# Kernel optimization log

Hardware: AMD Instinct MI355X
Metric: run time of the kernel (lower is better)

The kernel has to match this reference:

```python
import jax, jax.numpy as jnp
import numpy as np

B, N = 2048, 1024
GRAVITY = 9.81007
SIG_G2 = (1.6968e-4) ** 2  # default gyro covariance (EuRoC)
SIG_A2 = (2.0e-3) ** 2     # default accel covariance (EuRoC)


def skew(v):
    x, y, z = v[..., 0], v[..., 1], v[..., 2]
    o = jnp.zeros_like(x)
    return jnp.stack([
        jnp.stack([o, -z, y], -1),
        jnp.stack([z, o, -x], -1),
        jnp.stack([-y, x, o], -1)], -2)


def so3_exp(phi):
    # phi [...,3] -> unit quaternion [...,4] (xyzw)
    t2 = jnp.sum(phi * phi, axis=-1, keepdims=True)
    small = t2 < 1e-8
    t = jnp.sqrt(jnp.where(small, 1.0, t2))
    s = jnp.where(small, 0.5 - t2 / 48.0, jnp.sin(0.5 * t) / t)
    w = jnp.where(small, 1.0 - t2 / 8.0, jnp.cos(0.5 * t))
    return jnp.concatenate([phi * s, w], axis=-1)


def so3_Jr(phi):
    # right Jacobian of Exp at phi: I - c1*K + c2*K@K
    t2 = jnp.sum(phi * phi, axis=-1)[..., None, None]
    small = t2 < 1e-8
    t2s = jnp.where(small, 1.0, t2)
    t = jnp.sqrt(t2s)
    c1 = jnp.where(small, 0.5 - t2 / 24.0, (1.0 - jnp.cos(t)) / t2s)
    c2 = jnp.where(small, 1.0 / 6.0 - t2 / 120.0, (t - jnp.sin(t)) / (t2s * t))
    K = skew(phi)
    I = jnp.eye(3, dtype=phi.dtype)
    return I - c1 * K + c2 * (K @ K)


def quat_mul(q, r):
    x1, y1, z1, w1 = q[..., 0], q[..., 1], q[..., 2], q[..., 3]
    x2, y2, z2, w2 = r[..., 0], r[..., 1], r[..., 2], r[..., 3]
    return jnp.stack([
        w1 * x2 + x1 * w2 + y1 * z2 - z1 * y2,
        w1 * y2 - x1 * z2 + y1 * w2 + z1 * x2,
        w1 * z2 + x1 * y2 - y1 * x2 + z1 * w2,
        w1 * w2 - x1 * x2 - y1 * y2 - z1 * z2], -1)


def quat_inv(q):
    return jnp.concatenate([-q[..., :3], q[..., 3:]], -1)


def quat_to_mat(q):
    x, y, z, w = q[..., 0], q[..., 1], q[..., 2], q[..., 3]
    r0 = jnp.stack([1 - 2 * (y * y + z * z), 2 * (x * y - z * w), 2 * (x * z + y * w)], -1)
    r1 = jnp.stack([2 * (x * y + z * w), 1 - 2 * (x * x + z * z), 2 * (y * z - x * w)], -1)
    r2 = jnp.stack([2 * (x * z - y * w), 2 * (y * z + x * w), 1 - 2 * (x * x + y * y)], -1)
    return jnp.stack([r0, r1, r2], -2)


def rotate(q, v):
    return jnp.einsum('...ij,...j->...i', quat_to_mat(q), v)


def setup_inputs() -> dict:
    key = jax.random.key(0)
    k1, k2, k3 = jax.random.split(key, 3)
    dt = jax.random.uniform(k1, (B, N, 1), dtype=jnp.float32) * 0.004 + 0.001  # ~200Hz IMU
    ang = 0.5 * jax.random.normal(k2, (B, N, 3), dtype=jnp.float32)
    acc = jax.random.normal(k3, (B, N, 3), dtype=jnp.float32)
    pos0 = jnp.zeros((B, 3), jnp.float32)
    vel0 = jnp.zeros((B, 3), jnp.float32)
    rot0 = jnp.zeros((B, 4), jnp.float32).at[:, 3].set(1.0)  # identity SO3
    return {"dt": dt, "ang": ang, "acc": acc, "pos0": pos0, "vel0": vel0, "rot0": rot0}


def reference(dt, ang, acc, pos0, vel0, rot0):
    dtype = dt.dtype
    b = pos0.shape[0]
    grav = jnp.array([0.0, 0.0, GRAVITY], dtype=dtype)
    I3 = jnp.eye(3, dtype=dtype)

    def step(carry, x):
        dp, dv, drq, tacc, cov = carry
        dt_k, ang_k, acc_k = x  # [B,1], [B,3], [B,3]
        phi = ang_k * dt_k
        dr = so3_exp(phi)
        # a = acc - (rot0 * dr_ik * dr).Inv() @ gravity
        q_tot = quat_mul(quat_mul(rot0, drq), dr)
        a = acc_k - rotate(quat_inv(q_tot), grav)
        Ra = rotate(drq, a)  # old dR applied to a
        dp_n = dp + dv * dt_k + 0.5 * Ra * dt_k ** 2
        dv_n = dv + Ra * dt_k
        drq_n = quat_mul(drq, dr)
        tacc_n = tacc + dt_k
        # --- covariance propagation (Forster A7-A10) ---
        dtb = dt_k[..., None]             # [B,1,1]
        Rnew = quat_to_mat(drq_n)         # [B,3,3] (code uses updated dR)
        RHa = Rnew @ skew(acc_k)
        Z3 = jnp.zeros_like(RHa)
        E3 = jnp.broadcast_to(I3, RHa.shape)
        drT = jnp.swapaxes(quat_to_mat(dr), -1, -2)
        row0 = jnp.concatenate([drT, Z3, Z3], -1)
        row1 = jnp.concatenate([-RHa * dtb, E3, Z3], -1)
        row2 = jnp.concatenate([-0.5 * RHa * dtb ** 2, E3 * dtb, E3], -1)
        A = jnp.concatenate([row0, row1, row2], -2)  # [B,9,9]
        JrDt = so3_Jr(phi) * dtb
        Bg = jnp.concatenate([JrDt, Z3, Z3], -2)                              # [B,9,3]
        Ba = jnp.concatenate([Z3, Rnew * dtb, 0.5 * Rnew * dtb ** 2], -2)     # [B,9,3]
        cov_n = (A @ cov @ jnp.swapaxes(A, -1, -2)
                 + SIG_G2 * (Bg @ jnp.swapaxes(Bg, -1, -2))
                 + SIG_A2 * (Ba @ jnp.swapaxes(Ba, -1, -2)))
        return (dp_n, dv_n, drq_n, tacc_n, cov_n), None

    init = (jnp.zeros((b, 3), dtype), jnp.zeros((b, 3), dtype),
            jnp.tile(jnp.array([0.0, 0.0, 0.0, 1.0], dtype), (b, 1)),
            jnp.zeros((b, 1), dtype), jnp.zeros((b, 9, 9), dtype))
    xs = (jnp.swapaxes(dt, 0, 1), jnp.swapaxes(ang, 0, 1), jnp.swapaxes(acc, 0, 1))
    (dp, dv, drq, tacc, cov), _ = jax.lax.scan(step, init, xs)

    rot_out = quat_mul(rot0, drq)
    vel_out = vel0 + rotate(rot0, dv)
    pos_out = pos0 + vel0 * tacc + rotate(rot0, dp)
    return rot_out, vel_out, pos_out, cov
```

## Files before the change

### kernel.cpp

```cpp
#include <hip/hip_runtime.h>
#include <math.h>

#define GRAVITY_C 9.81007f
#define SIG_G2_C (1.6968e-4f * 1.6968e-4f)
#define SIG_A2_C (2.0e-3f * 2.0e-3f)

struct Seg {
  float q[4];
  float t;
  float dv[3], dp[3];
  float P10[9], P20[9];
  float c00[6], c01[9], c02[9], c11[6], c12[9], c22[6];
};

static __device__ __forceinline__ void q2m(const float q[4], float R[9]) {
  float x = q[0], y = q[1], z = q[2], w = q[3];
  R[0] = 1.f - 2.f * (y * y + z * z); R[1] = 2.f * (x * y - z * w);       R[2] = 2.f * (x * z + y * w);
  R[3] = 2.f * (x * y + z * w);       R[4] = 1.f - 2.f * (x * x + z * z); R[5] = 2.f * (y * z - x * w);
  R[6] = 2.f * (x * z - y * w);       R[7] = 2.f * (y * z + x * w);       R[8] = 1.f - 2.f * (x * x + y * y);
}

static __device__ __forceinline__ void qmul(const float a[4], const float b[4], float o[4]) {
  float x1 = a[0], y1 = a[1], z1 = a[2], w1 = a[3];
  float x2 = b[0], y2 = b[1], z2 = b[2], w2 = b[3];
  o[0] = w1 * x2 + x1 * w2 + y1 * z2 - z1 * y2;
  o[1] = w1 * y2 - x1 * z2 + y1 * w2 + z1 * x2;
  o[2] = w1 * z2 + x1 * y2 - y1 * x2 + z1 * w2;
  o[3] = w1 * w2 - x1 * x2 - y1 * y2 - z1 * z2;
}

static __device__ __forceinline__ void mm(const float A[9], const float B[9], float C[9]) {
#pragma unroll
  for (int i = 0; i < 3; i++)
#pragma unroll
    for (int j = 0; j < 3; j++)
      C[3 * i + j] = A[3 * i + 0] * B[0 + j] + A[3 * i + 1] * B[3 + j] + A[3 * i + 2] * B[6 + j];
}
static __device__ __forceinline__ void mmT(const float A[9], const float B[9], float C[9]) {
#pragma unroll
  for (int i = 0; i < 3; i++)
#pragma unroll
    for (int j = 0; j < 3; j++)
      C[3 * i + j] = A[3 * i + 0] * B[3 * j + 0] + A[3 * i + 1] * B[3 * j + 1] + A[3 * i + 2] * B[3 * j + 2];
}
static __device__ __forceinline__ void mTm(const float A[9], const float B[9], float C[9]) {
#pragma unroll
  for (int i = 0; i < 3; i++)
#pragma unroll
    for (int j = 0; j < 3; j++)
      C[3 * i + j] = A[0 + i] * B[0 + j] + A[3 + i] * B[3 + j] + A[6 + i] * B[6 + j];
}

static __device__ __forceinline__ void expand6(const float c[6], float f[9]) {
  f[0] = c[0]; f[1] = c[1]; f[2] = c[2];
  f[3] = c[1]; f[4] = c[3]; f[5] = c[4];
  f[6] = c[2]; f[7] = c[4]; f[8] = c[5];
}

__device__ __constant__ const int SI6[6] = {0, 0, 0, 1, 1, 2};
__device__ __constant__ const int SJ6[6] = {0, 1, 2, 1, 2, 2};

static __device__ __forceinline__ void step(Seg& s, float Ro[9], float gb[3], float dtv,
                                            float omx, float omy, float omz,
                                            float acx, float acy, float acz) {
  float px = omx * dtv, py = omy * dtv, pz = omz * dtv;
  float t2 = px * px + py * py + pz * pz;
  float s_ = 0.5f - t2 * (1.0f / 48.0f);
  float qd[4] = {px * s_, py * s_, pz * s_, 1.0f - 0.125f * t2};

  float Rd[9]; q2m(qd, Rd);
  float qn[4]; qmul(s.q, qd, qn);
  float Rn[9]; q2m(qn, Rn);

  float gbn[3];
#pragma unroll
  for (int i = 0; i < 3; i++)
    gbn[i] = Rd[0 + i] * gb[0] + Rd[3 + i] * gb[1] + Rd[6 + i] * gb[2];
  float bx = acx - gbn[0], by = acy - gbn[1], bz = acz - gbn[2];
  float Ra[3];
#pragma unroll
  for (int i = 0; i < 3; i++)
    Ra[i] = Ro[3 * i + 0] * bx + Ro[3 * i + 1] * by + Ro[3 * i + 2] * bz;

  float hdt = 0.5f * dtv;
  float hdt2 = hdt * dtv;
#pragma unroll
  for (int i = 0; i < 3; i++) s.dp[i] += s.dv[i] * dtv + Ra[i] * hdt2;
#pragma unroll
  for (int i = 0; i < 3; i++) s.dv[i] += Ra[i] * dtv;

  float M[9];
#pragma unroll
  for (int i = 0; i < 3; i++) {
    M[3 * i + 0] = -dtv * (Rn[3 * i + 1] * acz - Rn[3 * i + 2] * acy);
    M[3 * i + 1] = -dtv * (-Rn[3 * i + 0] * acz + Rn[3 * i + 2] * acx);
    M[3 * i + 2] = -dtv * (Rn[3 * i + 0] * acy - Rn[3 * i + 1] * acx);
  }

  float TP[9]; mmT(M, Ro, TP);
#pragma unroll
  for (int k = 0; k < 9; k++) s.P20[k] += hdt * TP[k] + dtv * s.P10[k];
#pragma unroll
  for (int k = 0; k < 9; k++) s.P10[k] += TP[k];

  float C00f[9]; expand6(s.c00, C00f);

  float W01[9]; mmT(C00f, TP, W01);
  float Y1h[9]; mm(TP, s.c01, Y1h);
  float Y2h[9]; mm(TP, s.c02, Y2h);

  float Wm6[6];
#pragma unroll
  for (int s6 = 0; s6 < 6; s6++) {
    const int i = SI6[s6], j = SJ6[s6];
    Wm6[s6] = W01[0 + i] * TP[3 * j + 0] + W01[3 + i] * TP[3 * j + 1] + W01[6 + i] * TP[3 * j + 2];
  }
  float WmF[9]; expand6(Wm6, WmF);

#pragma unroll
  for (int k = 0; k < 9; k++) s.c02[k] += hdt * (W01[k] + 2.0f * s.c01[k]);
#pragma unroll
  for (int k = 0; k < 9; k++) s.c01[k] += W01[k];

  {
    float ph[3];
#pragma unroll
    for (int i = 0; i < 3; i++)
      ph[i] = Rn[3 * i + 0] * px + Rn[3 * i + 1] * py + Rn[3 * i + 2] * pz;
    float sgdt2 = SIG_G2_C * dtv * dtv;
    float a_ = sgdt2 * (1.0f - t2 * (1.0f / 12.0f));
    float b_ = sgdt2 * ((1.0f / 12.0f) - t2 * (1.0f / 36.0f));
#pragma unroll
    for (int s6 = 0; s6 < 6; s6++) {
      const int i = SI6[s6], j = SJ6[s6];
      float v = s.c00[s6] + b_ * ph[i] * ph[j];
      if (i == j) v += a_;
      s.c00[s6] = v;
    }
  }

  float C11f[9]; expand6(s.c11, C11f);
  float c11p[9];
#pragma unroll
  for (int i = 0; i < 3; i++)
#pragma unroll
    for (int j = 0; j < 3; j++)
      c11p[3 * i + j] = WmF[3 * i + j] + Y1h[3 * i + j] + Y1h[3 * j + i] + C11f[3 * i + j];

  float c12p[9];
#pragma unroll
  for (int i = 0; i < 3; i++)
#pragma unroll
    for (int j = 0; j < 3; j++)
      c12p[3 * i + j] = hdt * (c11p[3 * i + j] + Y1h[3 * i + j] + C11f[3 * i + j])
                      + Y2h[3 * i + j] + s.c12[3 * i + j];

  float dt2v = dtv * dtv;
  float nh2 = -hdt * hdt;
#pragma unroll
  for (int s6 = 0; s6 < 6; s6++) {
    const int i = SI6[s6], j = SJ6[s6];
    float v = s.c22[s6]
            + hdt * (c12p[3 * i + j] + c12p[3 * j + i] + s.c12[3 * i + j] + s.c12[3 * j + i])
            + nh2 * (c11p[3 * i + j] - C11f[3 * i + j]);
    if (i == j) v += SIG_A2_C * 0.25f * dt2v * dt2v;
    s.c22[s6] = v;
  }
#pragma unroll
  for (int i = 0; i < 3; i++)
#pragma unroll
    for (int j = 0; j < 3; j++) {
      float v = c12p[3 * i + j];
      if (i == j) v += SIG_A2_C * hdt * dt2v;
      s.c12[3 * i + j] = v;
    }
#pragma unroll
  for (int s6 = 0; s6 < 6; s6++) {
    const int i = SI6[s6], j = SJ6[s6];
    float v = c11p[3 * i + j];
    if (i == j) v += SIG_A2_C * dt2v;
    s.c11[s6] = v;
  }

#pragma unroll
  for (int i = 0; i < 4; i++) s.q[i] = qn[i];
#pragma unroll
  for (int k = 0; k < 9; k++) Ro[k] = Rn[k];
#pragma unroll
  for (int i = 0; i < 3; i++) gb[i] = gbn[i];
  s.t += dtv;
}

template <int CNT>
static __device__ __forceinline__ void shsel(const float* v, int d, bool rt, float* X, float* Y) {
#pragma unroll
  for (int i = 0; i < CNT; i++) {
    float o = __shfl_xor(v[i], d, 64);
    X[i] = rt ? o : v[i];
    Y[i] = rt ? v[i] : o;
  }
}

static __device__ __forceinline__ void compose(Seg& s, int d, int lane) {
  bool rt = (lane & d) != 0;

  {
    float xq[4], yq[4];
    shsel<4>(s.q, d, rt, xq, yq);
    qmul(xq, yq, s.q);
  }
  float ot = __shfl_xor(s.t, d, 64);
  float tY = rt ? s.t : ot;
  s.t = s.t + ot;

  {
    float xu[3], yu[3], xw[3], yw[3];
    shsel<3>(s.dv, d, rt, xu, yu);
    shsel<3>(s.dp, d, rt, xw, yw);
#pragma unroll
    for (int i = 0; i < 3; i++) s.dp[i] = xw[i] + tY * xu[i] + yw[i];
#pragma unroll
    for (int i = 0; i < 3; i++) s.dv[i] = xu[i] + yu[i];
  }

  float N1[9], N2[9], xP10[9], xP20[9];
  shsel<9>(s.P10, d, rt, xP10, N1);
  shsel<9>(s.P20, d, rt, xP20, N2);

  float x00[6], y00[6];
  shsel<6>(s.c00, d, rt, x00, y00);
  float X00f[9]; expand6(x00, X00f);
  float K1[9]; mm(N1, X00f, K1);
  float K2[9]; mm(N2, X00f, K2);
#pragma unroll
  for (int s6 = 0; s6 < 6; s6++) s.c00[s6] = x00[s6] + y00[s6];

  float x01[9], y01[9];
  shsel<9>(s.c01, d, rt, x01, y01);
  float L1[9]; mm(N1, x01, L1);
  float L2[9]; mm(N2, x01, L2);
  float x02[9], y02[9];
  shsel<9>(s.c02, d, rt, x02, y02);
  float L3[9]; mm(N1, x02, L3);
  float L4[9]; mm(N2, x02, L4);

#pragma unroll
  for (int i = 0; i < 3; i++)
#pragma unroll
    for (int j = 0; j < 3; j++) {
      s.c01[3 * i + j] = x01[3 * i + j] + K1[3 * j + i] + y01[3 * i + j];
      s.c02[3 * i + j] = x02[3 * i + j] + tY * x01[3 * i + j] + K2[3 * j + i] + y02[3 * i + j];
    }

  float x11[6], y11[6], x12[9], y12[9], x22[6], y22[6];
  shsel<6>(s.c11, d, rt, x11, y11);
  shsel<9>(s.c12, d, rt, x12, y12);
  shsel<6>(s.c22, d, rt, x22, y22);
  float X11f[9]; expand6(x11, X11f);

#pragma unroll
  for (int s6 = 0; s6 < 6; s6++) {
    const int i = SI6[s6], j = SJ6[s6];
    float kn = K1[3 * i + 0] * N1[3 * j + 0] + K1[3 * i + 1] * N1[3 * j + 1] + K1[3 * i + 2] * N1[3 * j + 2];
    s.c11[s6] = x11[s6] + L1[3 * i + j] + L1[3 * j + i] + kn + y11[s6];
  }
#pragma unroll
  for (int i = 0; i < 3; i++)
#pragma unroll
    for (int j = 0; j < 3; j++) {
      float kn = K1[3 * i + 0] * N2[3 * j + 0] + K1[3 * i + 1] * N2[3 * j + 1] + K1[3 * i + 2] * N2[3 * j + 2];
      s.c12[3 * i + j] = x12[3 * i + j] + L3[3 * i + j] + tY * (L1[3 * i + j] + X11f[3 * i + j])
                       + L2[3 * j + i] + kn + y12[3 * i + j];
    }
  float tY2 = tY * tY;
#pragma unroll
  for (int s6 = 0; s6 < 6; s6++) {
    const int i = SI6[s6], j = SJ6[s6];
    float kn = K2[3 * i + 0] * N2[3 * j + 0] + K2[3 * i + 1] * N2[3 * j + 1] + K2[3 * i + 2] * N2[3 * j + 2];
    s.c22[s6] = x22[s6] + kn + L4[3 * i + j] + L4[3 * j + i]
              + tY * (L2[3 * i + j] + L2[3 * j + i] + x12[3 * i + j] + x12[3 * j + i])
              + tY2 * X11f[3 * i + j] + y22[s6];
  }

#pragma unroll
  for (int k = 0; k < 9; k++) s.P20[k] = xP20[k] + tY * xP10[k] + N2[k];
#pragma unroll
  for (int k = 0; k < 9; k++) s.P10[k] = xP10[k] + N1[k];
}

static __device__ __forceinline__ void sandw(const float R[9], float A[9]) {
  float T1[9]; mm(R, A, T1);
  mmT(T1, R, A);
}

__global__ __launch_bounds__(256, 1) void imu_kernel(
    const float* __restrict__ dt, const float* __restrict__ ang, const float* __restrict__ acc,
    const float* __restrict__ pos0, const float* __restrict__ vel0, const float* __restrict__ rot0,
    float* __restrict__ out, int B, int N) {
  int lane = threadIdx.x & 63;
  int wave = threadIdx.x >> 6;
  int b = blockIdx.x * 4 + wave;
  if (b >= B) return;
  int chunk = N >> 6;

  long base = (long)b * N + (long)lane * chunk;
  const float* dtp = dt + base;
  const float* angp = ang + base * 3;
  const float* accp = acc + base * 3;

  float qc[4] = {0.f, 0.f, 0.f, 1.f};
#pragma unroll 1
  for (int jb = 0; jb < (chunk >> 2); ++jb) {
    float4 d4 = *reinterpret_cast<const float4*>(dtp + jb * 4);
    float4 g0 = *reinterpret_cast<const float4*>(angp + jb * 12 + 0);
    float4 g1 = *reinterpret_cast<const float4*>(angp + jb * 12 + 4);
    float4 g2 = *reinterpret_cast<const float4*>(angp + jb * 12 + 8);
    float dd[4] = {d4.x, d4.y, d4.z, d4.w};
    float gg[12] = {g0.x, g0.y, g0.z, g0.w, g1.x, g1.y, g1.z, g1.w, g2.x, g2.y, g2.z, g2.w};
#pragma unroll
    for (int u = 0; u < 4; ++u) {
      float dtv = dd[u];
      float px = gg[3 * u + 0] * dtv, py = gg[3 * u + 1] * dtv, pz = gg[3 * u + 2] * dtv;
      float t2 = px * px + py * py + pz * pz;
      float s_ = 0.5f - t2 * (1.0f / 48.0f);
      float qd[4] = {px * s_, py * s_, pz * s_, 1.0f - 0.125f * t2};
      float qn[4]; qmul(qc, qd, qn);
      qc[0] = qn[0]; qc[1] = qn[1]; qc[2] = qn[2]; qc[3] = qn[3];
    }
  }
#pragma unroll
  for (int d = 1; d < 64; d <<= 1) {
    float o0 = __shfl_up(qc[0], d, 64);
    float o1 = __shfl_up(qc[1], d, 64);
    float o2 = __shfl_up(qc[2], d, 64);
    float o3 = __shfl_up(qc[3], d, 64);
    if (lane >= d) {
      float oq[4] = {o0, o1, o2, o3};
      float nn[4]; qmul(oq, qc, nn);
      qc[0] = nn[0]; qc[1] = nn[1]; qc[2] = nn[2]; qc[3] = nn[3];
    }
  }
  float Q[4];
  Q[0] = __shfl_up(qc[0], 1, 64);
  Q[1] = __shfl_up(qc[1], 1, 64);
  Q[2] = __shfl_up(qc[2], 1, 64);
  Q[3] = __shfl_up(qc[3], 1, 64);
  if (lane == 0) { Q[0] = 0.f; Q[1] = 0.f; Q[2] = 0.f; Q[3] = 1.f; }

  float RQ[9]; q2m(Q, RQ);

  float r0q[4] = {rot0[b * 4 + 0], rot0[b * 4 + 1], rot0[b * 4 + 2], rot0[b * 4 + 3]};
  float g_l[3];
  {
    float R0[9]; q2m(r0q, R0);
    float gp[3] = {R0[6] * GRAVITY_C, R0[7] * GRAVITY_C, R0[8] * GRAVITY_C};
#pragma unroll
    for (int i = 0; i < 3; i++)
      g_l[i] = RQ[0 + i] * gp[0] + RQ[3 + i] * gp[1] + RQ[6 + i] * gp[2];
  }

  Seg s = {};
  s.q[3] = 1.0f;
  float Ro[9] = {1.f, 0.f, 0.f, 0.f, 1.f, 0.f, 0.f, 0.f, 1.f};
  float gb[3] = {g_l[0], g_l[1], g_l[2]};

  float dc = dtp[0];
  float gx = angp[0], gy = angp[1], gz = angp[2];
  float ax = accp[0], ay = accp[1], az = accp[2];
#pragma unroll 1
  for (int j = 0; j < chunk; ++j) {
    int jn = (j + 1 < chunk) ? j + 1 : j;
    float dn = dtp[jn];
    float gnx = angp[3 * jn + 0], gny = angp[3 * jn + 1], gnz = angp[3 * jn + 2];
    float anx = accp[3 * jn + 0], any2 = accp[3 * jn + 1], anz = accp[3 * jn + 2];
    step(s, Ro, gb, dc, gx, gy, gz, ax, ay, az);
    dc = dn; gx = gnx; gy = gny; gz = gnz; ax = anx; ay = any2; az = anz;
  }

  {
    float tv[3];
#pragma unroll
    for (int i = 0; i < 3; i++)
      tv[i] = RQ[3 * i + 0] * s.dv[0] + RQ[3 * i + 1] * s.dv[1] + RQ[3 * i + 2] * s.dv[2];
#pragma unroll
    for (int i = 0; i < 3; i++) s.dv[i] = tv[i];
#pragma unroll
    for (int i = 0; i < 3; i++)
      tv[i] = RQ[3 * i + 0] * s.dp[0] + RQ[3 * i + 1] * s.dp[1] + RQ[3 * i + 2] * s.dp[2];
#pragma unroll
    for (int i = 0; i < 3; i++) s.dp[i] = tv[i];
    sandw(RQ, s.P10);
    sandw(RQ, s.P20);
    sandw(RQ, s.c01);
    sandw(RQ, s.c02);
    sandw(RQ, s.c12);
    float F[9];
    expand6(s.c00, F); sandw(RQ, F);
    s.c00[0] = F[0]; s.c00[1] = F[1]; s.c00[2] = F[2]; s.c00[3] = F[4]; s.c00[4] = F[5]; s.c00[5] = F[8];
    expand6(s.c11, F); sandw(RQ, F);
    s.c11[0] = F[0]; s.c11[1] = F[1]; s.c11[2] = F[2]; s.c11[3] = F[4]; s.c11[4] = F[5]; s.c11[5] = F[8];
    expand6(s.c22, F); sandw(RQ, F);
    s.c22[0] = F[0]; s.c22[1] = F[1]; s.c22[2] = F[2]; s.c22[3] = F[4]; s.c22[4] = F[5]; s.c22[5] = F[8];
  }

#pragma unroll 1
  for (int d = 1; d < 64; d <<= 1) compose(s, d, lane);

  if (lane == 0) {
    float p0[3] = {pos0[b * 3 + 0], pos0[b * 3 + 1], pos0[b * 3 + 2]};
    float v0[3] = {vel0[b * 3 + 0], vel0[b * 3 + 1], vel0[b * 3 + 2]};
    float R0[9]; q2m(r0q, R0);
    float qo[4]; qmul(r0q, s.q, qo);
#pragma unroll
    for (int i = 0; i < 4; i++) out[b * 4 + i] = qo[i];
#pragma unroll
    for (int i = 0; i < 3; i++) {
      float vv = v0[i] + R0[3 * i + 0] * s.dv[0] + R0[3 * i + 1] * s.dv[1] + R0[3 * i + 2] * s.dv[2];
      float pv = p0[i] + v0[i] * s.t + R0[3 * i + 0] * s.dp[0] + R0[3 * i + 1] * s.dp[1] + R0[3 * i + 2] * s.dp[2];
      out[4 * B + b * 3 + i] = vv;
      out[7 * B + b * 3 + i] = pv;
    }
    float Rq[9]; q2m(s.q, Rq);
    float C00f[9];
    {
      float G[9]; expand6(s.c00, G);
      float T1[9]; mTm(Rq, G, T1);
      mm(T1, Rq, C00f);
    }
    float C01f[9]; mTm(Rq, s.c01, C01f);
    float C02f[9]; mTm(Rq, s.c02, C02f);
    float C11f[9], C22f[9];
    expand6(s.c11, C11f); expand6(s.c22, C22f);

    long cb = 10L * B + (long)b * 81;
#pragma unroll
    for (int i = 0; i < 3; i++)
#pragma unroll
      for (int j = 0; j < 3; j++) {
        out[cb + i * 9 + j]           = C00f[3 * i + j];
        out[cb + i * 9 + (j + 3)]     = C01f[3 * i + j];
        out[cb + i * 9 + (j + 6)]     = C02f[3 * i + j];
        out[cb + (i + 3) * 9 + j]     = C01f[3 * j + i];
        out[cb + (i + 3) * 9 + j + 3] = C11f[3 * i + j];
        out[cb + (i + 3) * 9 + j + 6] = s.c12[3 * i + j];
        out[cb + (i + 6) * 9 + j]     = C02f[3 * j + i];
        out[cb + (i + 6) * 9 + j + 3] = s.c12[3 * j + i];
        out[cb + (i + 6) * 9 + j + 6] = C22f[3 * i + j];
      }
  }
}

extern "C" void kernel_launch(void* const* d_in, const int* in_sizes, int n_in,
                              void* d_out, int out_size, void* d_ws, size_t ws_size,
                              hipStream_t stream) {
  const float* dt   = (const float*)d_in[0];
  const float* ang  = (const float*)d_in[1];
  const float* acc  = (const float*)d_in[2];
  const float* pos0 = (const float*)d_in[3];
  const float* vel0 = (const float*)d_in[4];
  const float* rot0 = (const float*)d_in[5];
  int B = in_sizes[5] / 4;
  int N = in_sizes[0] / B;
  float* out = (float*)d_out;
  dim3 grid((B + 3) / 4), block(256);
  imu_kernel<<<grid, block, 0, stream>>>(dt, ang, acc, pos0, vel0, rot0, out, B, N);
}
```

Baseline: 76.93 us.

## Replace pairwise segment composition with suffix scan plus butterfly sum

```diff
diff --git a/kernel.cpp b/kernel.cpp
--- a/kernel.cpp
+++ b/kernel.cpp
@@ -104,7 +104,6 @@
   for (int k = 0; k < 9; k++) s.P10[k] += TP[k];
 
   float C00f[9]; expand6(s.c00, C00f);
-
   float W01[9]; mmT(C00f, TP, W01);
   float Y1h[9]; mm(TP, s.c01, Y1h);
   float Y2h[9]; mm(TP, s.c02, Y2h);
@@ -191,106 +190,14 @@
   s.t += dtv;
 }
 
-template <int CNT>
-static __device__ __forceinline__ void shsel(const float* v, int d, bool rt, float* X, float* Y) {
-#pragma unroll
-  for (int i = 0; i < CNT; i++) {
-    float o = __shfl_xor(v[i], d, 64);
-    X[i] = rt ? o : v[i];
-    Y[i] = rt ? v[i] : o;
-  }
-}
-
-static __device__ __forceinline__ void compose(Seg& s, int d, int lane) {
-  bool rt = (lane & d) != 0;
-
-  {
-    float xq[4], yq[4];
-    shsel<4>(s.q, d, rt, xq, yq);
-    qmul(xq, yq, s.q);
-  }
-  float ot = __shfl_xor(s.t, d, 64);
-  float tY = rt ? s.t : ot;
-  s.t = s.t + ot;
-
-  {
-    float xu[3], yu[3], xw[3], yw[3];
-    shsel<3>(s.dv, d, rt, xu, yu);
-    shsel<3>(s.dp, d, rt, xw, yw);
-#pragma unroll
-    for (int i = 0; i < 3; i++) s.dp[i] = xw[i] + tY * xu[i] + yw[i];
-#pragma unroll
-    for (int i = 0; i < 3; i++) s.dv[i] = xu[i] + yu[i];
-  }
-
-  float N1[9], N2[9], xP10[9], xP20[9];
-  shsel<9>(s.P10, d, rt, xP10, N1);
-  shsel<9>(s.P20, d, rt, xP20, N2);
-
-  float x00[6], y00[6];
-  shsel<6>(s.c00, d, rt, x00, y00);
-  float X00f[9]; expand6(x00, X00f);
-  float K1[9]; mm(N1, X00f, K1);
-  float K2[9]; mm(N2, X00f, K2);
-#pragma unroll
-  for (int s6 = 0; s6 < 6; s6++) s.c00[s6] = x00[s6] + y00[s6];
-
-  float x01[9], y01[9];
-  shsel<9>(s.c01, d, rt, x01, y01);
-  float L1[9]; mm(N1, x01, L1);
-  float L2[9]; mm(N2, x01, L2);
-  float x02[9], y02[9];
-  shsel<9>(s.c02, d, rt, x02, y02);
-  float L3[9]; mm(N1, x02, L3);
-  float L4[9]; mm(N2, x02, L4);
-
-#pragma unroll
-  for (int i = 0; i < 3; i++)
-#pragma unroll
-    for (int j = 0; j < 3; j++) {
-      s.c01[3 * i + j] = x01[3 * i + j] + K1[3 * j + i] + y01[3 * i + j];
-      s.c02[3 * i + j] = x02[3 * i + j] + tY * x01[3 * i + j] + K2[3 * j + i] + y02[3 * i + j];
-    }
-
-  float x11[6], y11[6], x12[9], y12[9], x22[6], y22[6];
-  shsel<6>(s.c11, d, rt, x11, y11);
-  shsel<9>(s.c12, d, rt, x12, y12);
-  shsel<6>(s.c22, d, rt, x22, y22);
-  float X11f[9]; expand6(x11, X11f);
-
-#pragma unroll
-  for (int s6 = 0; s6 < 6; s6++) {
-    const int i = SI6[s6], j = SJ6[s6];
-    float kn = K1[3 * i + 0] * N1[3 * j + 0] + K1[3 * i + 1] * N1[3 * j + 1] + K1[3 * i + 2] * N1[3 * j + 2];
-    s.c11[s6] = x11[s6] + L1[3 * i + j] + L1[3 * j + i] + kn + y11[s6];
-  }
-#pragma unroll
-  for (int i = 0; i < 3; i++)
-#pragma unroll
-    for (int j = 0; j < 3; j++) {
-      float kn = K1[3 * i + 0] * N2[3 * j + 0] + K1[3 * i + 1] * N2[3 * j + 1] + K1[3 * i + 2] * N2[3 * j + 2];
-      s.c12[3 * i + j] = x12[3 * i + j] + L3[3 * i + j] + tY * (L1[3 * i + j] + X11f[3 * i + j])
-                       + L2[3 * j + i] + kn + y12[3 * i + j];
-    }
-  float tY2 = tY * tY;
-#pragma unroll
-  for (int s6 = 0; s6 < 6; s6++) {
-    const int i = SI6[s6], j = SJ6[s6];
-    float kn = K2[3 * i + 0] * N2[3 * j + 0] + K2[3 * i + 1] * N2[3 * j + 1] + K2[3 * i + 2] * N2[3 * j + 2];
-    s.c22[s6] = x22[s6] + kn + L4[3 * i + j] + L4[3 * j + i]
-              + tY * (L2[3 * i + j] + L2[3 * j + i] + x12[3 * i + j] + x12[3 * j + i])
-              + tY2 * X11f[3 * i + j] + y22[s6];
-  }
-
-#pragma unroll
-  for (int k = 0; k < 9; k++) s.P20[k] = xP20[k] + tY * xP10[k] + N2[k];
-#pragma unroll
-  for (int k = 0; k < 9; k++) s.P10[k] = xP10[k] + N1[k];
-}
-
 static __device__ __forceinline__ void sandw(const float R[9], float A[9]) {
   float T1[9]; mm(R, A, T1);
   mmT(T1, R, A);
+}
+
+static __device__ __forceinline__ float shdn(float v, int d, bool ok) {
+  float o = __shfl_down(v, d, 64);
+  return ok ? o : 0.0f;
 }
 
 __global__ __launch_bounds__(256, 1) void imu_kernel(
@@ -340,6 +247,11 @@
       qc[0] = nn[0]; qc[1] = nn[1]; qc[2] = nn[2]; qc[3] = nn[3];
     }
   }
+  float qT[4];
+  qT[0] = __shfl(qc[0], 63, 64);
+  qT[1] = __shfl(qc[1], 63, 64);
+  qT[2] = __shfl(qc[2], 63, 64);
+  qT[3] = __shfl(qc[3], 63, 64);
   float Q[4];
   Q[0] = __shfl_up(qc[0], 1, 64);
   Q[1] = __shfl_up(qc[1], 1, 64);
@@ -347,16 +259,18 @@
   Q[3] = __shfl_up(qc[3], 1, 64);
   if (lane == 0) { Q[0] = 0.f; Q[1] = 0.f; Q[2] = 0.f; Q[3] = 1.f; }
 
-  float RQ[9]; q2m(Q, RQ);
-
-  float r0q[4] = {rot0[b * 4 + 0], rot0[b * 4 + 1], rot0[b * 4 + 2], rot0[b * 4 + 3]};
   float g_l[3];
   {
+    float r0q[4] = {rot0[b * 4 + 0], rot0[b * 4 + 1], rot0[b * 4 + 2], rot0[b * 4 + 3]};
     float R0[9]; q2m(r0q, R0);
     float gp[3] = {R0[6] * GRAVITY_C, R0[7] * GRAVITY_C, R0[8] * GRAVITY_C};
-#pragma unroll
-    for (int i = 0; i < 3; i++)
-      g_l[i] = RQ[0 + i] * gp[0] + RQ[3 + i] * gp[1] + RQ[6 + i] * gp[2];
+    float qx = -Q[0], qy = -Q[1], qz = -Q[2], qw = Q[3];
+    float tx = 2.0f * (qy * gp[2] - qz * gp[1]);
+    float ty = 2.0f * (qz * gp[0] - qx * gp[2]);
+    float tz = 2.0f * (qx * gp[1] - qy * gp[0]);
+    g_l[0] = gp[0] + qw * tx + (qy * tz - qz * ty);
+    g_l[1] = gp[1] + qw * ty + (qz * tx - qx * tz);
+    g_l[2] = gp[2] + qw * tz + (qx * ty - qy * tx);
   }
 
   Seg s = {};
@@ -378,6 +292,7 @@
   }
 
   {
+    float RQ[9]; q2m(Q, RQ);
     float tv[3];
 #pragma unroll
     for (int i = 0; i < 3; i++)
@@ -403,14 +318,103 @@
     s.c22[0] = F[0]; s.c22[1] = F[1]; s.c22[2] = F[2]; s.c22[3] = F[4]; s.c22[4] = F[5]; s.c22[5] = F[8];
   }
 
-#pragma unroll 1
-  for (int d = 1; d < 64; d <<= 1) compose(s, d, lane);
+  float S1[9], S2[9], Tt;
+  {
+    bool ok0 = lane < 63;
+#pragma unroll
+    for (int k = 0; k < 9; k++) {
+      S1[k] = shdn(s.P10[k], 1, ok0);
+      S2[k] = shdn(s.P20[k], 1, ok0);
+    }
+    Tt = shdn(s.t, 1, ok0);
+#pragma unroll
+    for (int d = 1; d < 64; d <<= 1) {
+      bool ok = (lane + d) < 64;
+      float fT = shdn(Tt, d, ok);
+      float fS1[9], fS2[9];
+#pragma unroll
+      for (int k = 0; k < 9; k++) { fS1[k] = shdn(S1[k], d, ok); fS2[k] = shdn(S2[k], d, ok); }
+#pragma unroll
+      for (int k = 0; k < 9; k++) S2[k] = fS2[k] + fT * S1[k] + S2[k];
+#pragma unroll
+      for (int k = 0; k < 9; k++) S1[k] += fS1[k];
+      Tt += fT;
+    }
+  }
+
+  {
+    float A9[9]; expand6(s.c00, A9);
+    float ASt[9]; mmT(A9, S1, ASt);
+    float AZt[9]; mmT(A9, S2, AZt);
+    float SB[9];  mm(S1, s.c01, SB);
+    float ZB[9];  mm(S2, s.c01, ZB);
+    float ZC[9];  mm(S2, s.c02, ZC);
+    float D9[9];  expand6(s.c11, D9);
+
+    float r02[9];
+#pragma unroll
+    for (int k = 0; k < 9; k++) r02[k] = AZt[k] + Tt * s.c01[k] + s.c02[k];
+    float Sr02[9]; mm(S1, r02, Sr02);
+
+    float r01[9];
+#pragma unroll
+    for (int k = 0; k < 9; k++) r01[k] = ASt[k] + s.c01[k];
+
+    float r11[6];
+#pragma unroll
+    for (int s6 = 0; s6 < 6; s6++) {
+      const int i = SI6[s6], j = SJ6[s6];
+      float sast = S1[3 * i + 0] * ASt[0 + j] + S1[3 * i + 1] * ASt[3 + j] + S1[3 * i + 2] * ASt[6 + j];
+      r11[s6] = sast + SB[3 * i + j] + SB[3 * j + i] + s.c11[s6];
+    }
+    float r22[6];
+#pragma unroll
+    for (int s6 = 0; s6 < 6; s6++) {
+      const int i = SI6[s6], j = SJ6[s6];
+      float zazt = S2[3 * i + 0] * AZt[0 + j] + S2[3 * i + 1] * AZt[3 + j] + S2[3 * i + 2] * AZt[6 + j];
+      r22[s6] = zazt + Tt * (ZB[3 * i + j] + ZB[3 * j + i]) + (ZC[3 * i + j] + ZC[3 * j + i])
+              + Tt * Tt * D9[3 * i + j] + Tt * (s.c12[3 * i + j] + s.c12[3 * j + i]) + s.c22[s6];
+    }
+    float r12[9];
+#pragma unroll
+    for (int i = 0; i < 3; i++)
+#pragma unroll
+      for (int j = 0; j < 3; j++)
+        r12[3 * i + j] = Sr02[3 * i + j] + ZB[3 * j + i] + Tt * D9[3 * i + j] + s.c12[3 * i + j];
+
+#pragma unroll
+    for (int k = 0; k < 9; k++) { s.c01[k] = r01[k]; s.c02[k] = r02[k]; s.c12[k] = r12[k]; }
+#pragma unroll
+    for (int s6 = 0; s6 < 6; s6++) { s.c11[s6] = r11[s6]; s.c22[s6] = r22[s6]; }
+#pragma unroll
+    for (int i = 0; i < 3; i++) s.dp[i] += Tt * s.dv[i];
+  }
+
+#pragma unroll
+  for (int d = 1; d < 64; d <<= 1) {
+#pragma unroll
+    for (int k = 0; k < 6; k++) s.c00[k] += __shfl_xor(s.c00[k], d, 64);
+#pragma unroll
+    for (int k = 0; k < 9; k++) s.c01[k] += __shfl_xor(s.c01[k], d, 64);
+#pragma unroll
+    for (int k = 0; k < 9; k++) s.c02[k] += __shfl_xor(s.c02[k], d, 64);
+#pragma unroll
+    for (int k = 0; k < 6; k++) s.c11[k] += __shfl_xor(s.c11[k], d, 64);
+#pragma unroll
+    for (int k = 0; k < 9; k++) s.c12[k] += __shfl_xor(s.c12[k], d, 64);
+#pragma unroll
+    for (int k = 0; k < 6; k++) s.c22[k] += __shfl_xor(s.c22[k], d, 64);
+#pragma unroll
+    for (int k = 0; k < 3; k++) { s.dv[k] += __shfl_xor(s.dv[k], d, 64); s.dp[k] += __shfl_xor(s.dp[k], d, 64); }
+    s.t += __shfl_xor(s.t, d, 64);
+  }
 
   if (lane == 0) {
+    float r0q[4] = {rot0[b * 4 + 0], rot0[b * 4 + 1], rot0[b * 4 + 2], rot0[b * 4 + 3]};
     float p0[3] = {pos0[b * 3 + 0], pos0[b * 3 + 1], pos0[b * 3 + 2]};
     float v0[3] = {vel0[b * 3 + 0], vel0[b * 3 + 1], vel0[b * 3 + 2]};
     float R0[9]; q2m(r0q, R0);
-    float qo[4]; qmul(r0q, s.q, qo);
+    float qo[4]; qmul(r0q, qT, qo);
 #pragma unroll
     for (int i = 0; i < 4; i++) out[b * 4 + i] = qo[i];
 #pragma unroll
@@ -420,7 +424,7 @@
       out[4 * B + b * 3 + i] = vv;
       out[7 * B + b * 3 + i] = pv;
     }
-    float Rq[9]; q2m(s.q, Rq);
+    float Rq[9]; q2m(qT, Rq);
     float C00f[9];
     {
       float G[9]; expand6(s.c00, G);
```

Result: faster. 71.29 us, median of 2 (-7.3%).
